# Performance work log

Measured on AMD Instinct MI355X. Metric: run time of the kernel, lower is better.

## Reference

```python
import jax, jax.numpy as jnp
import numpy as np

D = 512       # hidden size
L = 256       # decode length
B = 512       # batch
NL = 2        # num LSTM layers


def setup_inputs() -> dict:
    key = jax.random.key(0)
    ks = jax.random.split(key, 16)
    s = 1.0 / np.sqrt(D)

    def w(k, shape):
        return jax.random.uniform(k, shape, jnp.float32, -s, s)

    return {
        "c_star": jax.random.normal(ks[0], (B, D), jnp.float32),
        "init_h_w": w(ks[1], (NL * D, D)),
        "init_h_b": w(ks[2], (NL * D,)),
        "init_c_w": w(ks[3], (NL * D, D)),
        "init_c_b": w(ks[4], (NL * D,)),
        "W_ih0": w(ks[5], (4 * D, 1)),
        "W_hh0": w(ks[6], (4 * D, D)),
        "b_ih0": w(ks[7], (4 * D,)),
        "b_hh0": w(ks[8], (4 * D,)),
        "W_ih1": w(ks[9], (4 * D, D)),
        "W_hh1": w(ks[10], (4 * D, D)),
        "b_ih1": w(ks[11], (4 * D,)),
        "b_hh1": w(ks[12], (4 * D,)),
        "out_w": w(ks[13], (1, D)),
        "out_b": w(ks[14], (1,)),
    }


def _lstm_layer(xW, h0, c0, W_hh):
    # xW: [L, B, 4D] precomputed input contribution (W_ih x + b_ih + b_hh)
    def step(carry, xw):
        h, c = carry
        gates = xw + h @ W_hh.T                 # [B, 4D]
        i, f, g, o = jnp.split(gates, 4, axis=-1)  # torch gate order i,f,g,o
        c = jax.nn.sigmoid(f) * c + jax.nn.sigmoid(i) * jnp.tanh(g)
        h = jax.nn.sigmoid(o) * jnp.tanh(c)
        return (h, c), h

    _, ys = jax.lax.scan(step, (h0, c0), xW)
    return ys  # [L, B, D]


def reference(c_star, init_h_w, init_h_b, init_c_w, init_c_b,
              W_ih0, W_hh0, b_ih0, b_hh0,
              W_ih1, W_hh1, b_ih1, b_hh1,
              out_w, out_b):
    Bsz, d = c_star.shape
    # Faithful to torch: (B, NL*d) tensor .view(NL, B, d) = flat row-major reshape
    h0 = jnp.tanh(c_star @ init_h_w.T + init_h_b).reshape(NL, Bsz, d)
    c0 = jnp.tanh(c_star @ init_c_w.T + init_c_b).reshape(NL, Bsz, d)

    # Layer 0: input is all zeros -> input contribution is just the biases
    xW0 = jnp.broadcast_to(b_ih0 + b_hh0, (L, Bsz, 4 * d))
    y0 = _lstm_layer(xW0, h0[0], c0[0], W_hh0)          # [L, B, D]

    # Layer 1: input is layer-0 output (dropout inactive at inference)
    xW1 = jnp.einsum('lbd,hd->lbh', y0, W_ih1) + b_ih1 + b_hh1
    y1 = _lstm_layer(xW1, h0[1], c0[1], W_hh1)          # [L, B, D]

    Y = jnp.swapaxes(y1, 0, 1)                          # [B, L, D]
    O = (Y @ out_w.T + out_b)[..., 0]                   # [B, L]
    recon = O[:, :L - 1]
    pred = O[:, L - 1]
    return recon, pred
```

## Files before the change

### kernel.cpp

```cpp
#include <hip/hip_runtime.h>


typedef __bf16 bf16_t;
typedef __bf16 bf16x8 __attribute__((ext_vector_type(8)));
typedef float f32x4 __attribute__((ext_vector_type(4)));
typedef float f32x16 __attribute__((ext_vector_type(16)));

#define D_ 512
#define NB 256
#define TPB 256
#define SCOPE_DEV __HIP_MEMORY_SCOPE_AGENT

#define OFF_O        0u
#define OFF_CTR      524288u
#define OFF_HL0      528384u
#define OFF_HL1      1576960u
#define OFF_CL0      2625536u
#define OFF_CL1      3674112u
#define OFF_CSB      4722688u
#define OFF_IHWB     5246976u
#define OFF_ICWB     6295552u
#define OFF_WHH0B    7344128u
#define OFF_WHH1B    9441280u
#define OFF_WIH1P    11538432u
#define OFF_GB0      13635584u
#define OFF_GB1      13643776u
#define OFF_Y0       13651968u
#define OFF_OP       147869696u

__device__ __forceinline__ float sigm(float x) { return 1.0f / (1.0f + __expf(-x)); }
__device__ __forceinline__ float tanh_f(float x) { return 1.0f - 2.0f / (__expf(2.0f * x) + 1.0f); }

__device__ __forceinline__ bf16x8 ld16_dev(const bf16_t* p) {
    const unsigned long long* q = (const unsigned long long*)p;
    unsigned long long v0 = __hip_atomic_load(q, __ATOMIC_RELAXED, SCOPE_DEV);
    unsigned long long v1 = __hip_atomic_load(q + 1, __ATOMIC_RELAXED, SCOPE_DEV);
    union { unsigned long long u[2]; bf16x8 v; } c;
    c.u[0] = v0; c.u[1] = v1;
    return c.v;
}
__device__ __forceinline__ void st8_dev(bf16_t* p, unsigned long long v) {
    __hip_atomic_store((unsigned long long*)p, v, __ATOMIC_RELAXED, SCOPE_DEV);
}

__global__ void prep_kernel(const float* __restrict__ c_star, const float* __restrict__ ihw,
                            const float* __restrict__ icw, const float* __restrict__ whh0,
                            const float* __restrict__ whh1, const float* __restrict__ bi0,
                            const float* __restrict__ bh0, const float* __restrict__ bi1,
                            const float* __restrict__ bh1,
                            bf16_t* __restrict__ csb, bf16_t* __restrict__ ihwb,
                            bf16_t* __restrict__ icwb, bf16_t* __restrict__ whh0b,
                            bf16_t* __restrict__ whh1b, float* __restrict__ gb0,
                            float* __restrict__ gb1) {
    int id = blockIdx.x * TPB + threadIdx.x;
    if (id < 262144) { csb[id] = (bf16_t)c_star[id]; return; }
    id -= 262144;
    if (id < 524288) { ihwb[id] = (bf16_t)ihw[id]; return; }
    id -= 524288;
    if (id < 524288) { icwb[id] = (bf16_t)icw[id]; return; }
    id -= 524288;
    if (id < 1048576) { whh0b[id] = (bf16_t)whh0[id]; return; }
    id -= 1048576;
    if (id < 1048576) { whh1b[id] = (bf16_t)whh1[id]; return; }
    id -= 1048576;
    if (id < 2048) { gb0[id] = bi0[id] + bh0[id]; return; }
    id -= 2048;
    if (id < 2048) { gb1[id] = bi1[id] + bh1[id]; return; }
}

__global__ void pack_wih1_kernel(const float* __restrict__ W, bf16_t* __restrict__ out) {
    int id = blockIdx.x * TPB + threadIdx.x;
    int j = id >> 13;
    int ch = id & 8191;
    int c = ch >> 6;
    int k0 = (ch & 63) << 3;
    int q = c >> 5, dd = c & 31;
    int src = (q * 512 + j * 32 + dd) * 512 + k0;
    int kt = k0 >> 4, hi = (k0 >> 3) & 1;
    int off = (j * 4 + q) * 16384 + kt * 512 + ((hi << 5) + dd) * 8;
#pragma unroll
    for (int jj = 0; jj < 8; jj++) out[off + jj] = (bf16_t)W[src + jj];
}

__global__ __launch_bounds__(TPB) void init_gemm_kernel(
    const bf16_t* __restrict__ csb, const bf16_t* __restrict__ ihwb,
    const bf16_t* __restrict__ icwb, const float* __restrict__ ihb,
    const float* __restrict__ icb, bf16_t* __restrict__ hl0, bf16_t* __restrict__ hl1,
    float* __restrict__ cl0, float* __restrict__ cl1) {
    int bid = blockIdx.x;
    int mt = bid & 15, nt = bid >> 4;
    int tid = threadIdx.x;
    int w = tid >> 6, l = tid & 63;
    int lane32 = l & 31, lhi = l >> 5;
    int m0 = mt * 32;
    int n0 = nt * 128 + w * 32;
    bool is_h = (n0 < 1024);
    const bf16_t* Bmat = is_h ? ihwb : icwb;
    const float* bias = is_h ? ihb : icb;
    int nloc = is_h ? n0 : (n0 - 1024);

    f32x16 acc = {};
    const bf16_t* ap = csb + (m0 + lane32) * 512 + lhi * 8;
    const bf16_t* bp = Bmat + (nloc + lane32) * 512 + lhi * 8;
#pragma unroll
    for (int kt = 0; kt < 32; kt++) {
        bf16x8 a = *(const bf16x8*)(ap + kt * 16);
        bf16x8 b = *(const bf16x8*)(bp + kt * 16);
        acc = __builtin_amdgcn_mfma_f32_32x32x16_bf16(a, b, acc, 0, 0, 0);
    }
    int n = nloc + lane32;
    float bv = bias[n];
#pragma unroll
    for (int reg = 0; reg < 16; reg++) {
        int row = (reg & 3) + ((reg >> 2) << 3) + (lhi << 2);
        int m = m0 + row;
        float v = tanh_f(acc[reg] + bv);
        int flat = m * 1024 + n;
        if (is_h) {
            if (flat < 262144) hl0[flat] = (bf16_t)v;
            else hl1[flat - 262144] = (bf16_t)v;
        } else {
            if (flat < 262144) cl0[flat] = v;
            else cl1[flat - 262144] = v;
        }
    }
}

__global__ __launch_bounds__(TPB, 1) void lstm_main_kernel(
    const bf16_t* __restrict__ whh0, const bf16_t* __restrict__ whh1,
    const bf16_t* __restrict__ wih1p, const float* __restrict__ gb0,
    const float* __restrict__ gb1, const float* __restrict__ out_w,
    bf16_t* __restrict__ hl0, bf16_t* __restrict__ hl1,
    const float* __restrict__ cl0i, const float* __restrict__ cl1i,
    bf16_t* __restrict__ y0, float* __restrict__ OP, unsigned* __restrict__ flg) {
    __shared__ __align__(16) char smem[163840];
    bf16_t* Wlds = (bf16_t*)smem;
    float* P = (float*)(smem + 131072);

    const int bid = blockIdx.x;
    const int r8 = bid & 7, k8 = bid >> 3;
    const int g = r8 + ((k8 >> 4) << 3);
    const int j = k8 & 15;
    const int b0 = g * 32, d0 = j * 32;
    const int tid = threadIdx.x;
    const int w = tid >> 6, l = tid & 63;
    const int lane32 = l & 31, lhi = l >> 5;
    const int kh = w >> 1;
    const int q0 = (w & 1) << 1;
    const int prow = tid >> 3, pc4 = (tid & 7) << 2;
    unsigned* gflags = flg + g * 16;

    for (int ch = tid; ch < 8192; ch += TPB) {
        int c = ch >> 6, k0 = (ch & 63) << 3;
        int q = c >> 5, dd = c & 31;
        bf16x8 v = *(const bf16x8*)(whh0 + (q * 512 + d0 + dd) * 512 + k0);
        *(bf16x8*)(Wlds + q * 16384 + (k0 >> 4) * 512 + ((((k0 >> 3) & 1) << 5) + dd) * 8) = v;
    }
    __syncthreads();

    f32x4 cst = *(const f32x4*)(cl0i + (b0 + prow) * 512 + d0 + pc4);
    f32x4 bq[4];
#pragma unroll
    for (int q = 0; q < 4; q++) bq[q] = *(const f32x4*)(gb0 + q * 512 + d0 + pc4);

    int barcnt = 0;

    for (int t = 0; t < 256; t++) {
        const bf16_t* hcur = hl0 + (t & 1) * 262144;
        bf16_t* hnxt = hl0 + ((t + 1) & 1) * 262144;
        f32x16 acc0 = {}, acc1 = {};
        const bf16_t* ap = hcur + (b0 + lane32) * 512 + kh * 256 + lhi * 8;
        const bf16_t* bpA = Wlds + q0 * 16384 + kh * 16 * 512 + l * 8;
        const bf16_t* bpB = bpA + 16384;
#pragma unroll
        for (int kt = 0; kt < 16; kt++) {
            bf16x8 a = ld16_dev(ap + kt * 16);
            acc0 = __builtin_amdgcn_mfma_f32_32x32x16_bf16(a, *(const bf16x8*)(bpA + kt * 512), acc0, 0, 0, 0);
            acc1 = __builtin_amdgcn_mfma_f32_32x32x16_bf16(a, *(const bf16x8*)(bpB + kt * 512), acc1, 0, 0, 0);
        }
#pragma unroll
        for (int reg = 0; reg < 16; reg++) {
            int row = (reg & 3) + ((reg >> 2) << 3) + (lhi << 2);
            P[(kh * 4 + q0) * 1024 + row * 32 + lane32] = acc0[reg];
            P[(kh * 4 + q0 + 1) * 1024 + row * 32 + lane32] = acc1[reg];
        }
        __syncthreads();
        {
            int eo = prow * 32 + pc4;
            f32x4 gI = *(const f32x4*)(P + eo) + *(const f32x4*)(P + 4096 + eo);
            f32x4 gF = *(const f32x4*)(P + 1024 + eo) + *(const f32x4*)(P + 5120 + eo);
            f32x4 gG = *(const f32x4*)(P + 2048 + eo) + *(const f32x4*)(P + 6144 + eo);
            f32x4 gO = *(const f32x4*)(P + 3072 + eo) + *(const f32x4*)(P + 7168 + eo);
            union { bf16_t h[4]; unsigned long long u; } pk;
#pragma unroll
            for (int k = 0; k < 4; k++) {
                float iv = sigm(gI[k] + bq[0][k]);
                float fv = sigm(gF[k] + bq[1][k]);
                float gv = tanh_f(gG[k] + bq[2][k]);
                float ov = sigm(gO[k] + bq[3][k]);
                float cv = fv * cst[k] + iv * gv;
                cst[k] = cv;
                pk.h[k] = (bf16_t)(ov * tanh_f(cv));
            }
            int gi = (b0 + prow) * 512 + d0 + pc4;
            st8_dev(hnxt + gi, pk.u);
            st8_dev(y0 + t * 262144 + gi, pk.u);
        }
        asm volatile("s_waitcnt vmcnt(0)" ::: "memory");
        __syncthreads();
        barcnt++;
        if (tid == 0) __hip_atomic_store(gflags + j, (unsigned)barcnt, __ATOMIC_RELAXED, SCOPE_DEV);
        if (w == 0) {
            const unsigned tgt = (unsigned)barcnt;
            for (;;) {
                unsigned v = tgt;
                if (l < 16) v = __hip_atomic_load(gflags + l, __ATOMIC_RELAXED, SCOPE_DEV);
                if (__all((int)(v >= tgt))) break;
                __builtin_amdgcn_s_sleep(1);
            }
        }
        __syncthreads();
    }

    for (int ch = tid; ch < 8192; ch += TPB) {
        int c = ch >> 6, k0 = (ch & 63) << 3;
        int q = c >> 5, dd = c & 31;
        bf16x8 v = *(const bf16x8*)(whh1 + (q * 512 + d0 + dd) * 512 + k0);
        *(bf16x8*)(Wlds + q * 16384 + (k0 >> 4) * 512 + ((((k0 >> 3) & 1) << 5) + dd) * 8) = v;
    }
    __syncthreads();
    cst = *(const f32x4*)(cl1i + (b0 + prow) * 512 + d0 + pc4);
#pragma unroll
    for (int q = 0; q < 4; q++) bq[q] = *(const f32x4*)(gb1 + q * 512 + d0 + pc4);
    const f32x4 own = *(const f32x4*)(out_w + d0 + pc4);
    const bf16_t* wpA = wih1p + (j * 4 + q0) * 16384 + kh * 16 * 512 + l * 8;
    const bf16_t* wpB = wpA + 16384;
    float* opj = OP + j * 131072;

    f32x16 yacc0 = {}, yacc1 = {};
    {
        const bf16_t* yp = y0 + (b0 + lane32) * 512 + kh * 256 + lhi * 8;
#pragma unroll
        for (int kt = 0; kt < 16; kt++) {
            bf16x8 a = *(const bf16x8*)(yp + kt * 16);
            yacc0 = __builtin_amdgcn_mfma_f32_32x32x16_bf16(a, *(const bf16x8*)(wpA + kt * 512), yacc0, 0, 0, 0);
            yacc1 = __builtin_amdgcn_mfma_f32_32x32x16_bf16(a, *(const bf16x8*)(wpB + kt * 512), yacc1, 0, 0, 0);
        }
    }

    for (int t = 0; t < 256; t++) {
        const bf16_t* hcur = hl1 + (t & 1) * 262144;
        bf16_t* hnxt = hl1 + ((t + 1) & 1) * 262144;
        f32x16 acc0 = yacc0, acc1 = yacc1;
        {
            const bf16_t* ap = hcur + (b0 + lane32) * 512 + kh * 256 + lhi * 8;
            const bf16_t* bpA = Wlds + q0 * 16384 + kh * 16 * 512 + l * 8;
            const bf16_t* bpB = bpA + 16384;
#pragma unroll
            for (int kt = 0; kt < 16; kt++) {
                bf16x8 a = ld16_dev(ap + kt * 16);
                acc0 = __builtin_amdgcn_mfma_f32_32x32x16_bf16(a, *(const bf16x8*)(bpA + kt * 512), acc0, 0, 0, 0);
                acc1 = __builtin_amdgcn_mfma_f32_32x32x16_bf16(a, *(const bf16x8*)(bpB + kt * 512), acc1, 0, 0, 0);
            }
        }
#pragma unroll
        for (int reg = 0; reg < 16; reg++) {
            int row = (reg & 3) + ((reg >> 2) << 3) + (lhi << 2);
            P[(kh * 4 + q0) * 1024 + row * 32 + lane32] = acc0[reg];
            P[(kh * 4 + q0 + 1) * 1024 + row * 32 + lane32] = acc1[reg];
        }
        __syncthreads();
        {
            int eo = prow * 32 + pc4;
            f32x4 gI = *(const f32x4*)(P + eo) + *(const f32x4*)(P + 4096 + eo);
            f32x4 gF = *(const f32x4*)(P + 1024 + eo) + *(const f32x4*)(P + 5120 + eo);
            f32x4 gG = *(const f32x4*)(P + 2048 + eo) + *(const f32x4*)(P + 6144 + eo);
            f32x4 gO = *(const f32x4*)(P + 3072 + eo) + *(const f32x4*)(P + 7168 + eo);
            union { bf16_t h[4]; unsigned long long u; } pk;
            float part = 0.0f;
#pragma unroll
            for (int k = 0; k < 4; k++) {
                float iv = sigm(gI[k] + bq[0][k]);
                float fv = sigm(gF[k] + bq[1][k]);
                float gv = tanh_f(gG[k] + bq[2][k]);
                float ov = sigm(gO[k] + bq[3][k]);
                float cv = fv * cst[k] + iv * gv;
                cst[k] = cv;
                float hv = ov * tanh_f(cv);
                pk.h[k] = (bf16_t)hv;
                part += hv * own[k];
            }
#pragma unroll
            for (int off = 1; off < 8; off <<= 1) part += __shfl_xor(part, off, 8);
            if ((tid & 7) == 0) opj[t * 512 + b0 + prow] = part;
            st8_dev(hnxt + (b0 + prow) * 512 + d0 + pc4, pk.u);
        }
        asm volatile("s_waitcnt vmcnt(0)" ::: "memory");
        __syncthreads();
        barcnt++;
        if (tid == 0) __hip_atomic_store(gflags + j, (unsigned)barcnt, __ATOMIC_RELAXED, SCOPE_DEV);
        if (t < 255) {
            f32x16 yn0 = {}, yn1 = {};
            const bf16_t* yp = y0 + (t + 1) * 262144 + (b0 + lane32) * 512 + kh * 256 + lhi * 8;
#pragma unroll
            for (int kt = 0; kt < 16; kt++) {
                bf16x8 a = *(const bf16x8*)(yp + kt * 16);
                yn0 = __builtin_amdgcn_mfma_f32_32x32x16_bf16(a, *(const bf16x8*)(wpA + kt * 512), yn0, 0, 0, 0);
                yn1 = __builtin_amdgcn_mfma_f32_32x32x16_bf16(a, *(const bf16x8*)(wpB + kt * 512), yn1, 0, 0, 0);
            }
            yacc0 = yn0; yacc1 = yn1;
        }
        if (w == 0) {
            const unsigned tgt = (unsigned)barcnt;
            for (;;) {
                unsigned v = tgt;
                if (l < 16) v = __hip_atomic_load(gflags + l, __ATOMIC_RELAXED, SCOPE_DEV);
                if (__all((int)(v >= tgt))) break;
                __builtin_amdgcn_s_sleep(1);
            }
        }
        __syncthreads();
    }
}

__global__ void finalize_kernel(const float* __restrict__ OP, const float* __restrict__ out_b,
                                float* __restrict__ out) {
    int id = blockIdx.x * TPB + threadIdx.x;
    int t = id >> 9, b = id & 511;
    float v = out_b[0];
#pragma unroll
    for (int jj = 0; jj < 16; jj++) v += OP[jj * 131072 + id];
    if (t < 255) out[b * 255 + t] = v;
    else out[130560 + b] = v;
}

extern "C" void kernel_launch(void* const* d_in, const int* in_sizes, int n_in,
                              void* d_out, int out_size, void* d_ws, size_t ws_size,
                              hipStream_t stream) {
    const float* c_star = (const float*)d_in[0];
    const float* init_h_w = (const float*)d_in[1];
    const float* init_h_b = (const float*)d_in[2];
    const float* init_c_w = (const float*)d_in[3];
    const float* init_c_b = (const float*)d_in[4];
    const float* W_hh0 = (const float*)d_in[6];
    const float* b_ih0 = (const float*)d_in[7];
    const float* b_hh0 = (const float*)d_in[8];
    const float* W_ih1 = (const float*)d_in[9];
    const float* W_hh1 = (const float*)d_in[10];
    const float* b_ih1 = (const float*)d_in[11];
    const float* b_hh1 = (const float*)d_in[12];
    const float* out_w = (const float*)d_in[13];
    const float* out_b = (const float*)d_in[14];

    char* ws = (char*)d_ws;
    unsigned* flg = (unsigned*)(ws + OFF_CTR);
    bf16_t* hl0 = (bf16_t*)(ws + OFF_HL0);
    bf16_t* hl1 = (bf16_t*)(ws + OFF_HL1);
    float* cl0 = (float*)(ws + OFF_CL0);
    float* cl1 = (float*)(ws + OFF_CL1);
    bf16_t* csb = (bf16_t*)(ws + OFF_CSB);
    bf16_t* ihwb = (bf16_t*)(ws + OFF_IHWB);
    bf16_t* icwb = (bf16_t*)(ws + OFF_ICWB);
    bf16_t* whh0b = (bf16_t*)(ws + OFF_WHH0B);
    bf16_t* whh1b = (bf16_t*)(ws + OFF_WHH1B);
    bf16_t* wih1p = (bf16_t*)(ws + OFF_WIH1P);
    float* gb0 = (float*)(ws + OFF_GB0);
    float* gb1 = (float*)(ws + OFF_GB1);
    bf16_t* y0 = (bf16_t*)(ws + OFF_Y0);
    float* OP = (float*)(ws + OFF_OP);

    hipMemsetAsync(ws + OFF_CTR, 0, 4096, stream);

    prep_kernel<<<13328, TPB, 0, stream>>>(c_star, init_h_w, init_c_w, W_hh0, W_hh1,
                                           b_ih0, b_hh0, b_ih1, b_hh1,
                                           csb, ihwb, icwb, whh0b, whh1b, gb0, gb1);
    pack_wih1_kernel<<<512, TPB, 0, stream>>>(W_ih1, wih1p);
    init_gemm_kernel<<<256, TPB, 0, stream>>>(csb, ihwb, icwb, init_h_b, init_c_b,
                                              hl0, hl1, cl0, cl1);

    const bf16_t* a_whh0 = whh0b; const bf16_t* a_whh1 = whh1b;
    const bf16_t* a_wih1p = wih1p; const float* a_gb0 = gb0; const float* a_gb1 = gb1;
    const float* a_outw = out_w;
    bf16_t* a_hl0 = hl0; bf16_t* a_hl1 = hl1;
    const float* a_cl0 = cl0; const float* a_cl1 = cl1;
    bf16_t* a_y0 = y0; float* a_OP = OP; unsigned* a_flg = flg;
    void* args[] = {&a_whh0, &a_whh1, &a_wih1p, &a_gb0, &a_gb1, &a_outw,
                    &a_hl0, &a_hl1, &a_cl0, &a_cl1, &a_y0, &a_OP, &a_flg};
    hipLaunchCooperativeKernel((void*)lstm_main_kernel, dim3(NB), dim3(TPB), args, 0, stream);

    finalize_kernel<<<512, TPB, 0, stream>>>(OP, out_b, (float*)d_out);
}
```

Baseline: 4.171 ms.

## Split recurrent K-reduction across eight waves with two-phase LDS accumulation

Doubles the threads per block of the persistent LSTM kernel from 256 to 512, so eight waves each handle a quarter of the K dimension (8 MFMA steps instead of 16). Partial sums are combined in LDS in two phases: the first half of the waves store, then the second half add in. Only the first 256 threads run the gate nonlinearities and the stores. The aim is to shorten the serial per-step matmul latency on the critical path, at the cost of an extra block barrier and LDS read-modify-write per step.

```diff
diff --git a/kernel.cpp b/kernel.cpp
--- a/kernel.cpp
+++ b/kernel.cpp
@@ -9,6 +9,7 @@
 #define D_ 512
 #define NB 256
 #define TPB 256
+#define TPBM 512
 #define SCOPE_DEV __HIP_MEMORY_SCOPE_AGENT
 
 #define OFF_O        0u
@@ -126,7 +127,7 @@
     }
 }
 
-__global__ __launch_bounds__(TPB, 1) void lstm_main_kernel(
+__global__ __launch_bounds__(TPBM, 1) void lstm_main_kernel(
     const bf16_t* __restrict__ whh0, const bf16_t* __restrict__ whh1,
     const bf16_t* __restrict__ wih1p, const float* __restrict__ gb0,
     const float* __restrict__ gb1, const float* __restrict__ out_w,
@@ -145,12 +146,12 @@
     const int tid = threadIdx.x;
     const int w = tid >> 6, l = tid & 63;
     const int lane32 = l & 31, lhi = l >> 5;
-    const int kh = w >> 1;
+    const int qt = w >> 1;
     const int q0 = (w & 1) << 1;
     const int prow = tid >> 3, pc4 = (tid & 7) << 2;
     unsigned* gflags = flg + g * 16;
 
-    for (int ch = tid; ch < 8192; ch += TPB) {
+    for (int ch = tid; ch < 8192; ch += TPBM) {
         int c = ch >> 6, k0 = (ch & 63) << 3;
         int q = c >> 5, dd = c & 31;
         bf16x8 v = *(const bf16x8*)(whh0 + (q * 512 + d0 + dd) * 512 + k0);
@@ -158,10 +159,13 @@
     }
     __syncthreads();
 
-    f32x4 cst = *(const f32x4*)(cl0i + (b0 + prow) * 512 + d0 + pc4);
-    f32x4 bq[4];
-#pragma unroll
-    for (int q = 0; q < 4; q++) bq[q] = *(const f32x4*)(gb0 + q * 512 + d0 + pc4);
+    f32x4 cst = {};
+    f32x4 bq[4] = {};
+    if (tid < 256) {
+        cst = *(const f32x4*)(cl0i + (b0 + prow) * 512 + d0 + pc4);
+#pragma unroll
+        for (int q = 0; q < 4; q++) bq[q] = *(const f32x4*)(gb0 + q * 512 + d0 + pc4);
+    }
 
     int barcnt = 0;
 
@@ -169,23 +173,36 @@
         const bf16_t* hcur = hl0 + (t & 1) * 262144;
         bf16_t* hnxt = hl0 + ((t + 1) & 1) * 262144;
         f32x16 acc0 = {}, acc1 = {};
-        const bf16_t* ap = hcur + (b0 + lane32) * 512 + kh * 256 + lhi * 8;
-        const bf16_t* bpA = Wlds + q0 * 16384 + kh * 16 * 512 + l * 8;
+        const bf16_t* ap = hcur + (b0 + lane32) * 512 + qt * 128 + lhi * 8;
+        const bf16_t* bpA = Wlds + q0 * 16384 + qt * 4096 + l * 8;
         const bf16_t* bpB = bpA + 16384;
 #pragma unroll
-        for (int kt = 0; kt < 16; kt++) {
+        for (int kt = 0; kt < 8; kt++) {
             bf16x8 a = ld16_dev(ap + kt * 16);
             acc0 = __builtin_amdgcn_mfma_f32_32x32x16_bf16(a, *(const bf16x8*)(bpA + kt * 512), acc0, 0, 0, 0);
             acc1 = __builtin_amdgcn_mfma_f32_32x32x16_bf16(a, *(const bf16x8*)(bpB + kt * 512), acc1, 0, 0, 0);
         }
-#pragma unroll
-        for (int reg = 0; reg < 16; reg++) {
-            int row = (reg & 3) + ((reg >> 2) << 3) + (lhi << 2);
-            P[(kh * 4 + q0) * 1024 + row * 32 + lane32] = acc0[reg];
-            P[(kh * 4 + q0 + 1) * 1024 + row * 32 + lane32] = acc1[reg];
-        }
-        __syncthreads();
-        {
+        if (qt < 2) {
+#pragma unroll
+            for (int reg = 0; reg < 16; reg++) {
+                int row = (reg & 3) + ((reg >> 2) << 3) + (lhi << 2);
+                int o = qt * 4096 + q0 * 1024 + row * 32 + lane32;
+                P[o] = acc0[reg];
+                P[o + 1024] = acc1[reg];
+            }
+        }
+        __syncthreads();
+        if (qt >= 2) {
+#pragma unroll
+            for (int reg = 0; reg < 16; reg++) {
+                int row = (reg & 3) + ((reg >> 2) << 3) + (lhi << 2);
+                int o = (qt - 2) * 4096 + q0 * 1024 + row * 32 + lane32;
+                P[o] += acc0[reg];
+                P[o + 1024] += acc1[reg];
+            }
+        }
+        __syncthreads();
+        if (tid < 256) {
             int eo = prow * 32 + pc4;
             f32x4 gI = *(const f32x4*)(P + eo) + *(const f32x4*)(P + 4096 + eo);
             f32x4 gF = *(const f32x4*)(P + 1024 + eo) + *(const f32x4*)(P + 5120 + eo);
@@ -222,26 +239,29 @@
         __syncthreads();
     }
 
-    for (int ch = tid; ch < 8192; ch += TPB) {
+    for (int ch = tid; ch < 8192; ch += TPBM) {
         int c = ch >> 6, k0 = (ch & 63) << 3;
         int q = c >> 5, dd = c & 31;
         bf16x8 v = *(const bf16x8*)(whh1 + (q * 512 + d0 + dd) * 512 + k0);
         *(bf16x8*)(Wlds + q * 16384 + (k0 >> 4) * 512 + ((((k0 >> 3) & 1) << 5) + dd) * 8) = v;
     }
     __syncthreads();
-    cst = *(const f32x4*)(cl1i + (b0 + prow) * 512 + d0 + pc4);
-#pragma unroll
-    for (int q = 0; q < 4; q++) bq[q] = *(const f32x4*)(gb1 + q * 512 + d0 + pc4);
-    const f32x4 own = *(const f32x4*)(out_w + d0 + pc4);
-    const bf16_t* wpA = wih1p + (j * 4 + q0) * 16384 + kh * 16 * 512 + l * 8;
+    f32x4 own = {};
+    if (tid < 256) {
+        cst = *(const f32x4*)(cl1i + (b0 + prow) * 512 + d0 + pc4);
+#pragma unroll
+        for (int q = 0; q < 4; q++) bq[q] = *(const f32x4*)(gb1 + q * 512 + d0 + pc4);
+        own = *(const f32x4*)(out_w + d0 + pc4);
+    }
+    const bf16_t* wpA = wih1p + (j * 4 + q0) * 16384 + qt * 4096 + l * 8;
     const bf16_t* wpB = wpA + 16384;
     float* opj = OP + j * 131072;
 
     f32x16 yacc0 = {}, yacc1 = {};
     {
-        const bf16_t* yp = y0 + (b0 + lane32) * 512 + kh * 256 + lhi * 8;
-#pragma unroll
-        for (int kt = 0; kt < 16; kt++) {
+        const bf16_t* yp = y0 + (b0 + lane32) * 512 + qt * 128 + lhi * 8;
+#pragma unroll
+        for (int kt = 0; kt < 8; kt++) {
             bf16x8 a = *(const bf16x8*)(yp + kt * 16);
             yacc0 = __builtin_amdgcn_mfma_f32_32x32x16_bf16(a, *(const bf16x8*)(wpA + kt * 512), yacc0, 0, 0, 0);
             yacc1 = __builtin_amdgcn_mfma_f32_32x32x16_bf16(a, *(const bf16x8*)(wpB + kt * 512), yacc1, 0, 0, 0);
@@ -253,24 +273,37 @@
         bf16_t* hnxt = hl1 + ((t + 1) & 1) * 262144;
         f32x16 acc0 = yacc0, acc1 = yacc1;
         {
-            const bf16_t* ap = hcur + (b0 + lane32) * 512 + kh * 256 + lhi * 8;
-            const bf16_t* bpA = Wlds + q0 * 16384 + kh * 16 * 512 + l * 8;
+            const bf16_t* ap = hcur + (b0 + lane32) * 512 + qt * 128 + lhi * 8;
+            const bf16_t* bpA = Wlds + q0 * 16384 + qt * 4096 + l * 8;
             const bf16_t* bpB = bpA + 16384;
 #pragma unroll
-            for (int kt = 0; kt < 16; kt++) {
+            for (int kt = 0; kt < 8; kt++) {
                 bf16x8 a = ld16_dev(ap + kt * 16);
                 acc0 = __builtin_amdgcn_mfma_f32_32x32x16_bf16(a, *(const bf16x8*)(bpA + kt * 512), acc0, 0, 0, 0);
                 acc1 = __builtin_amdgcn_mfma_f32_32x32x16_bf16(a, *(const bf16x8*)(bpB + kt * 512), acc1, 0, 0, 0);
             }
         }
-#pragma unroll
-        for (int reg = 0; reg < 16; reg++) {
-            int row = (reg & 3) + ((reg >> 2) << 3) + (lhi << 2);
-            P[(kh * 4 + q0) * 1024 + row * 32 + lane32] = acc0[reg];
-            P[(kh * 4 + q0 + 1) * 1024 + row * 32 + lane32] = acc1[reg];
-        }
-        __syncthreads();
-        {
+        if (qt < 2) {
+#pragma unroll
+            for (int reg = 0; reg < 16; reg++) {
+                int row = (reg & 3) + ((reg >> 2) << 3) + (lhi << 2);
+                int o = qt * 4096 + q0 * 1024 + row * 32 + lane32;
+                P[o] = acc0[reg];
+                P[o + 1024] = acc1[reg];
+            }
+        }
+        __syncthreads();
+        if (qt >= 2) {
+#pragma unroll
+            for (int reg = 0; reg < 16; reg++) {
+                int row = (reg & 3) + ((reg >> 2) << 3) + (lhi << 2);
+                int o = (qt - 2) * 4096 + q0 * 1024 + row * 32 + lane32;
+                P[o] += acc0[reg];
+                P[o + 1024] += acc1[reg];
+            }
+        }
+        __syncthreads();
+        if (tid < 256) {
             int eo = prow * 32 + pc4;
             f32x4 gI = *(const f32x4*)(P + eo) + *(const f32x4*)(P + 4096 + eo);
             f32x4 gF = *(const f32x4*)(P + 1024 + eo) + *(const f32x4*)(P + 5120 + eo);
@@ -301,9 +334,9 @@
         if (tid == 0) __hip_atomic_store(gflags + j, (unsigned)barcnt, __ATOMIC_RELAXED, SCOPE_DEV);
         if (t < 255) {
             f32x16 yn0 = {}, yn1 = {};
-            const bf16_t* yp = y0 + (t + 1) * 262144 + (b0 + lane32) * 512 + kh * 256 + lhi * 8;
-#pragma unroll
-            for (int kt = 0; kt < 16; kt++) {
+            const bf16_t* yp = y0 + (t + 1) * 262144 + (b0 + lane32) * 512 + qt * 128 + lhi * 8;
+#pragma unroll
+            for (int kt = 0; kt < 8; kt++) {
                 bf16x8 a = *(const bf16x8*)(yp + kt * 16);
                 yn0 = __builtin_amdgcn_mfma_f32_32x32x16_bf16(a, *(const bf16x8*)(wpA + kt * 512), yn0, 0, 0, 0);
                 yn1 = __builtin_amdgcn_mfma_f32_32x32x16_bf16(a, *(const bf16x8*)(wpB + kt * 512), yn1, 0, 0, 0);
@@ -386,7 +419,7 @@
     bf16_t* a_y0 = y0; float* a_OP = OP; unsigned* a_flg = flg;
     void* args[] = {&a_whh0, &a_whh1, &a_wih1p, &a_gb0, &a_gb1, &a_outw,
                     &a_hl0, &a_hl1, &a_cl0, &a_cl1, &a_y0, &a_OP, &a_flg};
-    hipLaunchCooperativeKernel((void*)lstm_main_kernel, dim3(NB), dim3(TPB), args, 0, stream);
+    hipLaunchCooperativeKernel((void*)lstm_main_kernel, dim3(NB), dim3(TPBM), args, 0, stream);
 
     finalize_kernel<<<512, TPB, 0, stream>>>(OP, out_b, (float*)d_out);
 }
```

Result: no change. 4.129 ms (median of 2 runs) (-1.0%).
